# Kernel optimization log

Measured on AMD Instinct MI355X. Metric: run time of the kernel, lower is better.

The kernel has to match this reference:

```python
import jax, jax.numpy as jnp
import numpy as np

HEADS = 16
KERNEL_EPS = 1e-4  # performer_pytorch softmax_kernel eps
LN_EPS = 1e-5


def layernorm(x, g, b):
    m = jnp.mean(x, axis=-1, keepdims=True)
    v = jnp.var(x, axis=-1, keepdims=True)
    return (x - m) * jax.lax.rsqrt(v + LN_EPS) * g + b


def softmax_kernel(x, proj, is_query):
    # FAVOR+ positive random features (performer_pytorch softmax_kernel)
    d = x.shape[-1]
    m = proj.shape[0]
    xn = x * (d ** -0.25)                                   # data_normalizer * data
    dd = jnp.einsum('bhnd,md->bhnm', xn, proj)              # projected logits
    diag = 0.5 * jnp.sum(xn * xn, axis=-1, keepdims=True)   # ||x||^2/2 * normalizer^2
    if is_query:
        stab = jnp.max(dd, axis=-1, keepdims=True)
    else:
        stab = jnp.max(dd, axis=(-2, -1), keepdims=True)
    return (m ** -0.5) * (jnp.exp(dd - diag - stab) + KERNEL_EPS)


def favor_attention(x, proj, Wq, bq, Wk, bk, Wv, bv, Wo, bo):
    B, N, D = x.shape
    dh = D // HEADS

    def split(t):
        return t.reshape(B, N, HEADS, dh).transpose(0, 2, 1, 3)  # b h n d

    q = split(x @ Wq.T + bq)
    k = split(x @ Wk.T + bk)
    v = split(x @ Wv.T + bv)

    qp = softmax_kernel(q, proj, True)    # b h n m
    kp = softmax_kernel(k, proj, False)   # b h n m

    # non-causal linear attention: O(n*m*d)
    ksum = kp.sum(axis=2)                                    # b h m
    d_inv = 1.0 / jnp.einsum('bhnm,bhm->bhn', qp, ksum)      # b h n
    ctx = jnp.einsum('bhnm,bhnd->bhmd', kp, v)               # b h m d
    out = jnp.einsum('bhnm,bhmd,bhn->bhnd', qp, ctx, d_inv)  # b h n d

    out = out.transpose(0, 2, 1, 3).reshape(B, N, D)
    return out @ Wo.T + bo


def reference(x, proj, ln1_g, ln1_b, Wq, bq, Wk, bk, Wv, bv, Wo, bo,
              ln2_g, ln2_b, W1, b1, W2, b2):
    depth = proj.shape[0]
    for i in range(depth):
        h = layernorm(x, ln1_g[i], ln1_b[i])
        x = x + favor_attention(h, proj[i], Wq[i], bq[i], Wk[i], bk[i],
                                Wv[i], bv[i], Wo[i], bo[i])
        h = layernorm(x, ln2_g[i], ln2_b[i])
        x = x + (jax.nn.gelu(h @ W1[i].T + b1[i], approximate=False) @ W2[i].T + b2[i])
    return x


def _orthogonal_features(rng, m, d):
    # gaussian orthogonal random matrix, scaling=1 (rows scaled by sqrt(d))
    blocks = []
    for _ in range(m // d):
        qmat, _ = np.linalg.qr(rng.standard_normal((d, d)))
        blocks.append(qmat.T)
    return (np.sqrt(d) * np.concatenate(blocks, axis=0)).astype(np.float32)


def setup_inputs() -> dict:
    B, N, D, L, M, DH = 4, 2048, 1024, 4, 256, 64
    key = jax.random.key(0)
    ks = jax.random.split(key, 8)
    rng = np.random.default_rng(0)
    proj = jnp.asarray(np.stack([_orthogonal_features(rng, M, DH) for _ in range(L)]))
    s = 0.02
    return {
        'x': jax.random.normal(ks[0], (B, N, D), jnp.float32),
        'proj': proj,
        'ln1_g': jnp.ones((L, D), jnp.float32),
        'ln1_b': jnp.zeros((L, D), jnp.float32),
        'Wq': s * jax.random.normal(ks[1], (L, D, D), jnp.float32),
        'bq': jnp.zeros((L, D), jnp.float32),
        'Wk': s * jax.random.normal(ks[2], (L, D, D), jnp.float32),
        'bk': jnp.zeros((L, D), jnp.float32),
        'Wv': s * jax.random.normal(ks[3], (L, D, D), jnp.float32),
        'bv': jnp.zeros((L, D), jnp.float32),
        'Wo': s * jax.random.normal(ks[4], (L, D, D), jnp.float32),
        'bo': jnp.zeros((L, D), jnp.float32),
        'ln2_g': jnp.ones((L, D), jnp.float32),
        'ln2_b': jnp.zeros((L, D), jnp.float32),
        'W1': s * jax.random.normal(ks[5], (L, D, D), jnp.float32),
        'b1': jnp.zeros((L, D), jnp.float32),
        'W2': s * jax.random.normal(ks[6], (L, D, D), jnp.float32),
        'b2': jnp.zeros((L, D), jnp.float32),
    }
```

## Files before the change

kernel.cpp:

```cpp
#include <hip/hip_runtime.h>

#define B_    4
#define N_    2048
#define D_    1024
#define L_    4
#define M_    256
#define DH_   64
#define H_    16
#define BH_   64
#define ROWS_ 8192
#define WN_   1048576

typedef __bf16 bf16x8 __attribute__((ext_vector_type(8)));
typedef float  f32x4  __attribute__((ext_vector_type(4)));
typedef unsigned short u16;

__device__ __forceinline__ u16 f2b(float f){
  unsigned u = __float_as_uint(f);
  u += 0x7FFFu + ((u >> 16) & 1u);
  return (u16)(u >> 16);
}
__device__ __forceinline__ float b2f(u16 h){ return __uint_as_float(((unsigned)h) << 16); }
__device__ __forceinline__ unsigned fkey(float x){
  unsigned u = __float_as_uint(x);
  return (u & 0x80000000u) ? ~u : (u | 0x80000000u);
}
__device__ __forceinline__ float fdec(unsigned k){
  unsigned u = (k & 0x80000000u) ? (k ^ 0x80000000u) : ~k;
  return __uint_as_float(u);
}

__device__ __forceinline__ void gload16(const u16* g, u16* l){
  __builtin_amdgcn_global_load_lds(
      (const __attribute__((address_space(1))) void*)g,
      (__attribute__((address_space(3))) void*)l, 16, 0, 0);
}

__global__ __launch_bounds__(256) void wcvt_k(const float* __restrict__ s, u16* __restrict__ d, long n){
  long i = ((long)blockIdx.x*256 + threadIdx.x)*4;
  if (i+3 < n){
    float4 v = *(const float4*)(s+i);
    d[i]=f2b(v.x); d[i+1]=f2b(v.y); d[i+2]=f2b(v.z); d[i+3]=f2b(v.w);
  } else {
    for(long j=i;j<n;j++) d[j]=f2b(s[j]);
  }
}

__global__ __launch_bounds__(256) void wcvt2_k(const float* __restrict__ s, u16* __restrict__ dbase, long n){
  long i = ((long)blockIdx.x*256 + threadIdx.x)*4;
  if (i < n){
    float4 v = *(const float4*)(s+i);
    long l = i >> 20, j = i & (WN_-1);
    u16* d = dbase + l*(6l*WN_) + j;
    d[0]=f2b(v.x); d[1]=f2b(v.y); d[2]=f2b(v.z); d[3]=f2b(v.w);
  }
}

__global__ void fillf_k(float* o, long n, float v){
  long i=(long)blockIdx.x*256+threadIdx.x; if(i<n) o[i]=v;
}

__global__ __launch_bounds__(256) void ln_k(const float* __restrict__ x,
    const float* __restrict__ g, const float* __restrict__ bt, u16* __restrict__ h){
  int row = blockIdx.x, t = threadIdx.x;
  const float* xr = x + (long)row*D_;
  float4 v = *(const float4*)(xr + t*4);
  float s  = v.x+v.y+v.z+v.w;
  float ss = v.x*v.x+v.y*v.y+v.z*v.z+v.w*v.w;
  #pragma unroll
  for (int m=1;m<64;m<<=1){ s += __shfl_xor(s,m); ss += __shfl_xor(ss,m); }
  __shared__ float ps[4][2];
  int w=t>>6;
  if ((t&63)==0){ ps[w][0]=s; ps[w][1]=ss; }
  __syncthreads();
  s  = ps[0][0]+ps[1][0]+ps[2][0]+ps[3][0];
  ss = ps[0][1]+ps[1][1]+ps[2][1]+ps[3][1];
  float mean = s*(1.0f/D_);
  float rs = rsqrtf(ss*(1.0f/D_) - mean*mean + 1e-5f);
  int c=t*4;
  u16* hr = h + (long)row*D_;
  hr[c+0]=f2b((v.x-mean)*rs*g[c+0]+bt[c+0]);
  hr[c+1]=f2b((v.y-mean)*rs*g[c+1]+bt[c+1]);
  hr[c+2]=f2b((v.z-mean)*rs*g[c+2]+bt[c+2]);
  hr[c+3]=f2b((v.w-mean)*rs*g[c+3]+bt[c+3]);
}

__global__ __launch_bounds__(256) void vt_k(const u16* __restrict__ V, u16* __restrict__ Vt){
  __shared__ __align__(16) u16 ts[64][72];
  int t=threadIdx.x, z=blockIdx.y, n0=blockIdx.x*64;
  int b=z>>4, hh=z&15;
  {
    int row=t>>2, c16=(t&3)*16;
    const u16* src = V + ((long)b*N_ + n0+row)*D_ + hh*DH_ + c16;
    *(uint4*)&ts[row][c16]   = *(const uint4*)src;
    *(uint4*)&ts[row][c16+8] = *(const uint4*)(src+8);
  }
  __syncthreads();
  {
    int d=t>>2, nc=(t&3)*16;
    union { u16 u[16]; uint4 q[2]; } tmp;
    #pragma unroll
    for (int j=0;j<16;j++) tmp.u[j]=ts[nc+j][d];
    u16* dst = Vt + (long)z*DH_*N_ + (long)d*N_ + n0+nc;
    *(uint4*)dst = tmp.q[0];
    *(uint4*)(dst+8) = tmp.q[1];
  }
}

#define STAGE_PS(Ps, P) \
  _Pragma("unroll") \
  for (int i=0;i<8;i++){ \
    int c=threadIdx.x+i*256, row=c>>3, c8=c&7; \
    uint4 dv = *(const uint4*)((P) + row*64 + c8*8); \
    *(uint4*)((char*)(Ps) + (row<<7) + ((c8<<4)^((row&7)<<4))) = dv; \
  }
#define STAGE_XS(Xs, X, b, hh, n0) \
  _Pragma("unroll") \
  for (int i=0;i<2;i++){ \
    int c=threadIdx.x+i*256, row=c>>3, c8=c&7; \
    uint4 dv = *(const uint4*)((X) + ((long)(b)*N_ + (n0)+row)*D_ + (hh)*DH_ + c8*8); \
    *(uint4*)((char*)(Xs) + (row<<7) + ((c8<<4)^((row&7)<<4))) = dv; \
  }
#define STAGE_XS_DG(Xs, X, b, hh, n0, dgL) \
  _Pragma("unroll") \
  for (int i=0;i<2;i++){ \
    int c=threadIdx.x+i*256, row=c>>3, c8=c&7; \
    uint4 dv = *(const uint4*)((X) + ((long)(b)*N_ + (n0)+row)*D_ + (hh)*DH_ + c8*8); \
    *(uint4*)((char*)(Xs) + (row<<7) + ((c8<<4)^((row&7)<<4))) = dv; \
    const u16* pe=(const u16*)&dv; \
    float sq=0.f; \
    _Pragma("unroll") \
    for (int e=0;e<8;e++){ float xv=b2f(pe[e]); sq += xv*xv; } \
    sq += __shfl_xor(sq,1); sq += __shfl_xor(sq,2); sq += __shfl_xor(sq,4); \
    if ((threadIdx.x&7)==0) (dgL)[row]=sq*0.0625f; \
  }
#define DD_MFMA(acc, Xs, Ps, w, lr, lg) \
  _Pragma("unroll") \
  for (int ks=0;ks<2;ks++){ \
    bf16x8 aF[4], bF[4]; \
    _Pragma("unroll") \
    for (int mi=0;mi<4;mi++){ \
      int row=mi*16+(lr); \
      aF[mi]=*(const bf16x8*)((const char*)(Xs) + (row<<7) + ((((ks<<2)+(lg))<<4)^((row&7)<<4))); \
    } \
    _Pragma("unroll") \
    for (int ni=0;ni<4;ni++){ \
      int row=(w)*64+ni*16+(lr); \
      bF[ni]=*(const bf16x8*)((const char*)(Ps) + (row<<7) + ((((ks<<2)+(lg))<<4)^((row&7)<<4))); \
    } \
    _Pragma("unroll") \
    for (int mi=0;mi<4;mi++) \
      _Pragma("unroll") \
      for (int ni=0;ni<4;ni++) \
        acc[mi][ni]=__builtin_amdgcn_mfma_f32_16x16x32_bf16(aF[mi],bF[ni],acc[mi][ni],0,0,0); \
  }

__global__ __launch_bounds__(256) void ddstab_k(
    const u16* __restrict__ X, const u16* __restrict__ P,
    unsigned* __restrict__ sk, int zoff)
{
  __shared__ __align__(16) char smem[46080];
  u16* Ps=(u16*)smem; u16* Xs=(u16*)(smem+36864); float* rm=(float*)(smem+45056);
  int t=threadIdx.x, w=t>>6, lane=t&63, lr=lane&15, lg=lane>>4;
  int zg=blockIdx.y+zoff, n0=blockIdx.x*64;
  int b=zg>>4, hh=zg&15;
  STAGE_PS(Ps, P); STAGE_XS(Xs, X, b, hh, n0);
  __syncthreads();
  f32x4 acc[4][4];
  #pragma unroll
  for (int mi=0;mi<4;mi++)
    #pragma unroll
    for (int ni=0;ni<4;ni++) acc[mi][ni]=(f32x4){0.f,0.f,0.f,0.f};
  DD_MFMA(acc, Xs, Ps, w, lr, lg);
  float mx = acc[0][0][0];
  #pragma unroll
  for (int mi=0;mi<4;mi++)
    #pragma unroll
    for (int ni=0;ni<4;ni++)
      #pragma unroll
      for (int r=0;r<4;r++) mx=fmaxf(mx,acc[mi][ni][r]);
  #pragma unroll
  for (int m=1;m<64;m<<=1) mx = fmaxf(mx, __shfl_xor(mx,m));
  if (lane==0) rm[w]=mx;
  __syncthreads();
  const float SN = 0.35355339059327373f;
  if (t==0) atomicMax(sk+zg, fkey(SN*fmaxf(fmaxf(rm[0],rm[1]),fmaxf(rm[2],rm[3]))));
}

__global__ __launch_bounds__(256) void ddctx_k(
    const u16* __restrict__ Kb, const u16* __restrict__ P,
    const u16* __restrict__ Vt, const unsigned* __restrict__ sk,
    float* __restrict__ part, float* __restrict__ kspart, int zoff)
{
  __shared__ __align__(16) char smem[54784];
  u16* Ps = (u16*)smem;
  u16* Tr = (u16*)smem;
  u16* Xs = (u16*)(smem+36864);
  u16* Vs = (u16*)(smem+45056);
  float* dgL = (float*)(smem+54272);
  int t=threadIdx.x, w=t>>6, lane=t&63, lr=lane&15, lg=lane>>4;
  int zl=blockIdx.y, zg=zl+zoff, slot=blockIdx.x;
  int b=zg>>4, hh=zg&15;
  const float SN = 0.35355339059327373f;
  float stab = fdec(sk[zg]);

  f32x4 cacc[4][4];
  #pragma unroll
  for (int mi=0;mi<4;mi++)
    #pragma unroll
    for (int ni=0;ni<4;ni++) cacc[mi][ni]=(f32x4){0.f,0.f,0.f,0.f};
  float ksp[4]={0.f,0.f,0.f,0.f};

  for (int s=0;s<4;++s){
    int n0 = slot*256 + s*64;
    STAGE_PS(Ps, P); STAGE_XS_DG(Xs, Kb, b, hh, n0, dgL);
    {
      int d=t>>2, nc=(t&3)*16;
      const u16* src = Vt + (long)zg*DH_*N_ + (long)d*N_ + n0 + nc;
      *(uint4*)&Vs[d*72+nc]   = *(const uint4*)src;
      *(uint4*)&Vs[d*72+nc+8] = *(const uint4*)(src+8);
    }
    __syncthreads();
    f32x4 acc[4][4];
    #pragma unroll
    for (int mi=0;mi<4;mi++)
      #pragma unroll
      for (int ni=0;ni<4;ni++) acc[mi][ni]=(f32x4){0.f,0.f,0.f,0.f};
    DD_MFMA(acc, Xs, Ps, w, lr, lg);
    __syncthreads();
    #pragma unroll
    for (int mi=0;mi<4;mi++)
      #pragma unroll
      for (int ni=0;ni<4;ni++){
        int col = w*64+ni*16+lr;
        #pragma unroll
        for (int r=0;r<4;r++){
          int rw = mi*16+lg*4+r;
          float kp = 0.0625f*(expf(SN*acc[mi][ni][r] - dgL[rw] - stab) + 1e-4f);
          Tr[col*72+rw] = f2b(kp);
          ksp[ni] += kp;
        }
      }
    __syncthreads();
    #pragma unroll
    for (int ks=0;ks<2;ks++){
      bf16x8 aF[4], bF[4];
      #pragma unroll
      for (int mi=0;mi<4;mi++)
        aF[mi]=*(const bf16x8*)(Tr + (w*64+mi*16+lr)*72 + ks*32 + lg*8);
      #pragma unroll
      for (int ni=0;ni<4;ni++)
        bF[ni]=*(const bf16x8*)(Vs + (ni*16+lr)*72 + ks*32 + lg*8);
      #pragma unroll
      for (int mi=0;mi<4;mi++)
        #pragma unroll
        for (int ni=0;ni<4;ni++)
          cacc[mi][ni]=__builtin_amdgcn_mfma_f32_16x16x32_bf16(aF[mi],bF[ni],cacc[mi][ni],0,0,0);
    }
    __syncthreads();
  }
  #pragma unroll
  for (int ni=0;ni<4;ni++){
    ksp[ni] += __shfl_xor(ksp[ni],16);
    ksp[ni] += __shfl_xor(ksp[ni],32);
  }
  if (lane<16){
    float* kb_ = kspart + ((long)zl*8+slot)*256;
    #pragma unroll
    for (int ni=0;ni<4;ni++) kb_[w*64+ni*16+lane] = ksp[ni];
  }
  float* pb = part + ((long)zl*8+slot)*16384;
  #pragma unroll
  for (int mi=0;mi<4;mi++)
    #pragma unroll
    for (int ni=0;ni<4;ni++){
      int d = ni*16+lr;
      #pragma unroll
      for (int r=0;r<4;r++){
        int m = w*64+mi*16+lg*4+r;
        pb[m*64+d] = cacc[mi][ni][r];
      }
    }
}

__global__ __launch_bounds__(256) void ctxred2_k(
    const float* __restrict__ part, const float* __restrict__ kspart,
    u16* __restrict__ ctxT, float* __restrict__ ksm)
{
  int z = blockIdx.x, t = threadIdx.x;
  const float* pz = part + (long)z*8*16384;
  const float* kz = kspart + (long)z*8*256;
  float s=0.f;
  #pragma unroll
  for (int s8=0;s8<8;s8++) s += kz[s8*256+t];
  ksm[(long)z*256+t]=s;
  f32x4 r4[16];
  #pragma unroll
  for (int j=0;j<16;j++) r4[j] = *(const f32x4*)(pz + (long)t*64 + j*4);
  #pragma unroll
  for (int s8=1;s8<8;s8++){
    const float* ps = pz + (long)s8*16384 + (long)t*64;
    #pragma unroll
    for (int j=0;j<16;j++) r4[j] += *(const f32x4*)(ps + j*4);
  }
  u16 rb[64];
  #pragma unroll
  for (int j=0;j<16;j++){
    rb[j*4+0]=f2b(r4[j][0]); rb[j*4+1]=f2b(r4[j][1]);
    rb[j*4+2]=f2b(r4[j][2]); rb[j*4+3]=f2b(r4[j][3]);
  }
  __shared__ __align__(16) u16 TT[64][72];
  u16* co = ctxT + (long)z*16384;
  for (int c=0;c<4;c++){
    __syncthreads();
    if ((t>>6)==c){
      int r=t&63;
      #pragma unroll
      for (int j=0;j<64;j+=8) *(uint4*)&TT[r][j] = *(const uint4*)&rb[j];
    }
    __syncthreads();
    int d=t>>2, mq=(t&3)*16;
    union { u16 u[16]; uint4 q[2]; } tmp;
    #pragma unroll
    for (int j=0;j<16;j++) tmp.u[j]=TT[mq+j][d];
    *(uint4*)(co + d*256 + c*64 + mq)     = tmp.q[0];
    *(uint4*)(co + d*256 + c*64 + mq + 8) = tmp.q[1];
  }
}

__global__ __launch_bounds__(256) void ddq_attn_k(
    const u16* __restrict__ Qb, const u16* __restrict__ P,
    const float* __restrict__ ksm, const u16* __restrict__ ctxT,
    u16* __restrict__ at, int zoff)
{
  __shared__ __align__(16) char smem[46336];
  u16*   Ps  = (u16*)smem;
  u16*   qpL = (u16*)smem;
  float* rdot= (float*)(smem+33792);
  float* dnvs= (float*)(smem+34816);
  u16*   Xs  = (u16*)(smem+36864);
  float* rm  = (float*)(smem+45056);
  float* dgL = (float*)(smem+46080);
  int t=threadIdx.x, w=t>>6, lane=t&63, lr=lane&15, lg=lane>>4;
  int zl=blockIdx.y, zg=zl+zoff, n0=blockIdx.x*64;
  int b=zg>>4, hh=zg&15;
  const float SN = 0.35355339059327373f;

  STAGE_PS(Ps, P); STAGE_XS_DG(Xs, Qb, b, hh, n0, dgL);
  __syncthreads();
  f32x4 acc[4][4];
  #pragma unroll
  for (int mi=0;mi<4;mi++)
    #pragma unroll
    for (int ni=0;ni<4;ni++) acc[mi][ni]=(f32x4){0.f,0.f,0.f,0.f};
  DD_MFMA(acc, Xs, Ps, w, lr, lg);
  float rmx[4][4];
  #pragma unroll
  for (int mi=0;mi<4;mi++)
    #pragma unroll
    for (int r=0;r<4;r++){
      float v = acc[mi][0][r];
      #pragma unroll
      for (int ni=1;ni<4;ni++) v=fmaxf(v, acc[mi][ni][r]);
      #pragma unroll
      for (int m=1;m<16;m<<=1) v = fmaxf(v, __shfl_xor(v,m));
      rmx[mi][r]=v;
    }
  if (lr==0){
    #pragma unroll
    for (int mi=0;mi<4;mi++)
      #pragma unroll
      for (int r=0;r<4;r++) rm[w*64 + mi*16 + lg*4 + r] = rmx[mi][r];
  }
  __syncthreads();
  const float* ksz = ksm + (long)zl*256;
  float kcol[4];
  #pragma unroll
  for (int ni=0;ni<4;ni++) kcol[ni] = ksz[w*64+ni*16+lr];
  float rd[4][4];
  #pragma unroll
  for (int mi=0;mi<4;mi++)
    #pragma unroll
    for (int r=0;r<4;r++){
      int rw = mi*16+lg*4+r;
      float st = fmaxf(fmaxf(rm[rw],rm[64+rw]),fmaxf(rm[128+rw],rm[192+rw]));
      float dgv = dgL[rw];
      float rsum = 0.f;
      #pragma unroll
      for (int ni=0;ni<4;ni++){
        int col = w*64+ni*16+lr;
        float qpv = 0.0625f*(expf(SN*acc[mi][ni][r] - dgv - SN*st) + 1e-4f);
        qpL[rw*264+col] = f2b(qpv);
        rsum += qpv*kcol[ni];
      }
      rd[mi][r]=rsum;
    }
  #pragma unroll
  for (int mi=0;mi<4;mi++)
    #pragma unroll
    for (int r=0;r<4;r++){
      #pragma unroll
      for (int m=1;m<16;m<<=1) rd[mi][r] += __shfl_xor(rd[mi][r],m);
    }
  if (lr==0){
    #pragma unroll
    for (int mi=0;mi<4;mi++)
      #pragma unroll
      for (int r=0;r<4;r++) rdot[w*64 + mi*16+lg*4+r] = rd[mi][r];
  }
  __syncthreads();
  if (t<64) dnvs[t] = 1.0f/(rdot[t]+rdot[64+t]+rdot[128+t]+rdot[192+t]);
  __syncthreads();
  const u16* cz = ctxT + (long)zl*16384;
  f32x4 aacc[4];
  #pragma unroll
  for (int ni=0;ni<4;ni++) aacc[ni]=(f32x4){0.f,0.f,0.f,0.f};
  #pragma unroll
  for (int ks=0;ks<8;ks++){
    bf16x8 aF = *(const bf16x8*)(qpL + (w*16+lr)*264 + ks*32 + lg*8);
    #pragma unroll
    for (int ni=0;ni<4;ni++){
      bf16x8 bF = *(const bf16x8*)(cz + (ni*16+lr)*256 + ks*32 + lg*8);
      aacc[ni]=__builtin_amdgcn_mfma_f32_16x16x32_bf16(aF,bF,aacc[ni],0,0,0);
    }
  }
  #pragma unroll
  for (int ni=0;ni<4;ni++){
    #pragma unroll
    for (int r=0;r<4;r++){
      int n = n0 + w*16 + lg*4 + r;
      at[((long)b*N_ + n)*D_ + hh*64 + ni*16 + lr] = f2b(aacc[ni][r]*dnvs[w*16+lg*4+r]);
    }
  }
}

template<int BM,int BN,int WR,int WC,int EPI,bool XS>
__global__ __launch_bounds__(256) void gemm_k(
    const u16* __restrict__ A, int lda,
    const u16* __restrict__ W, int ldw,
    const float* __restrict__ bias, const float* __restrict__ biasK, const float* __restrict__ biasV,
    void* __restrict__ Cv, int ldc, int K)
{
  static_assert(WR*WC==4, "4 waves");
  constexpr int WM=BM/WR, WN=BN/WC, MI=WM/16, NI=WN/16;
  __shared__ __align__(16) u16 As[BM*64];
  __shared__ __align__(16) u16 Ws[BN*64];
  int t=threadIdx.x;
  int bx, by;
  if (XS){
    unsigned gx=gridDim.x, flat=blockIdx.y*gx+blockIdx.x;
    unsigned cpx=(gx*gridDim.y)>>3;
    unsigned s=(flat&7)*cpx + (flat>>3);
    bx = s % gx; by = s / gx;
  } else { bx = blockIdx.x; by = blockIdx.y; }
  const u16* Ab = A + (long)by*BM*lda;
  const u16* Wb = W + (long)bx*BN*ldw;
  int w=t>>6, lane=t&63, lr=lane&15, lg=lane>>4;
  int wr=w/WC, wc=w%WC;
  int srow=lane>>3, swcol=((lane&7)^srow)*8;
  f32x4 acc[MI][NI];
  #pragma unroll
  for (int mi=0;mi<MI;mi++)
    #pragma unroll
    for(int ni=0;ni<NI;ni++) acc[mi][ni]=(f32x4){0.f,0.f,0.f,0.f};

  for (int k0=0;k0<K;k0+=64){
    #pragma unroll
    for (int i=0;i<BM/32;i++){
      int rb=w*(BM/4)+i*8;
      gload16(Ab + (long)(rb+srow)*lda + k0 + swcol, As + rb*64);
    }
    #pragma unroll
    for (int i=0;i<BN/32;i++){
      int rb=w*(BN/4)+i*8;
      gload16(Wb + (long)(rb+srow)*ldw + k0 + swcol, Ws + rb*64);
    }
    __syncthreads();
    #pragma unroll
    for (int ks=0;ks<2;ks++){
      bf16x8 aF[MI], bF[NI];
      #pragma unroll
      for (int mi=0;mi<MI;mi++){
        int row=wr*WM+mi*16+lr;
        aF[mi]=*(const bf16x8*)((const char*)As + (row<<7) + ((((ks<<2)+lg)<<4)^((row&7)<<4)));
      }
      #pragma unroll
      for (int ni=0;ni<NI;ni++){
        int row=wc*WN+ni*16+lr;
        bF[ni]=*(const bf16x8*)((const char*)Ws + (row<<7) + ((((ks<<2)+lg)<<4)^((row&7)<<4)));
      }
      #pragma unroll
      for (int mi=0;mi<MI;mi++)
        #pragma unroll
        for (int ni=0;ni<NI;ni++)
          acc[mi][ni]=__builtin_amdgcn_mfma_f32_16x16x32_bf16(aF[mi],bF[ni],acc[mi][ni],0,0,0);
    }
    __syncthreads();
  }

  #pragma unroll
  for (int mi=0;mi<MI;mi++){
    #pragma unroll
    for (int ni=0;ni<NI;ni++){
      int col = bx*BN + wc*WN + ni*16 + lr;
      float bv = 0.0f;
      if (EPI==6){
        int seg = col>>10;
        const float* bp = (seg==0)?bias:((seg==1)?biasK:biasV);
        bv = bp[col&1023];
      } else if (EPI<=2){
        bv = bias[col];
      }
      #pragma unroll
      for (int r=0;r<4;r++){
        int row = by*BM + wr*WM + mi*16 + lg*4 + r;
        float v = acc[mi][ni][r];
        if (EPI==0){
          ((u16*)Cv)[(long)row*ldc + col] = f2b(v+bv);
        } else if (EPI==1){
          ((float*)Cv)[(long)row*ldc + col] += v+bv;
        } else if (EPI==2){
          float u=v+bv;
          ((u16*)Cv)[(long)row*ldc + col] = f2b(0.5f*u*(1.0f+erff(u*0.70710678118654752f)));
        } else {
          int seg = col>>10, c = col&1023;
          ((u16*)Cv)[(long)seg*((long)ROWS_*D_) + (long)row*D_ + c] = f2b(v+bv);
        }
      }
    }
  }
}

struct WS {
  u16 *wbuf, *pjb, *hb, *qb, *kb, *pbuf, *sh16, *ctxT;
  float *part, *kspart, *ksm; unsigned* sky;
  size_t total;
};
static WS plan_ws(char* base, int allW, int CH){
  WS w; size_t off=0;
  auto al=[&](size_t b)->char*{ char* p=base+off; off=(off+b+255)&~(size_t)255; return p; };
  const size_t TB=(size_t)ROWS_*D_*2;
  w.wbuf=(u16*)al((allW?6ull*L_:6ull)*WN_*2);
  w.pjb =(u16*)al((size_t)L_*M_*DH_*2);
  w.hb  =(u16*)al(TB);
  w.qb  =(u16*)al(TB);
  w.kb  =(u16*)al(TB);
  w.pbuf=(u16*)al(TB);
  w.sh16=(u16*)al(TB);
  w.part=(float*)al((size_t)CH*8*M_*DH_*4);
  w.kspart=(float*)al((size_t)CH*8*M_*4);
  w.ctxT=(u16*)al((size_t)BH_*DH_*M_*2);
  w.ksm =(float*)al((size_t)BH_*M_*4);
  w.sky =(unsigned*)al((size_t)L_*BH_*4);
  w.total=off;
  return w;
}

extern "C" void kernel_launch(void* const* d_in, const int* in_sizes, int n_in,
                              void* d_out, int out_size, void* d_ws, size_t ws_size,
                              hipStream_t stream)
{
  const float* x    = (const float*)d_in[0];
  const float* proj = (const float*)d_in[1];
  const float* ln1g = (const float*)d_in[2];
  const float* ln1b = (const float*)d_in[3];
  const float* Wq   = (const float*)d_in[4];
  const float* bq   = (const float*)d_in[5];
  const float* Wk   = (const float*)d_in[6];
  const float* bk   = (const float*)d_in[7];
  const float* Wv   = (const float*)d_in[8];
  const float* bv   = (const float*)d_in[9];
  const float* Wo   = (const float*)d_in[10];
  const float* bo   = (const float*)d_in[11];
  const float* ln2g = (const float*)d_in[12];
  const float* ln2b = (const float*)d_in[13];
  const float* W1   = (const float*)d_in[14];
  const float* b1   = (const float*)d_in[15];
  const float* W2   = (const float*)d_in[16];
  const float* b2   = (const float*)d_in[17];

  char* base=(char*)d_ws;
  int allW=1, CH=64;
  WS w = plan_ws(base, 1, 64);
  if (w.total > ws_size){ CH=16; w = plan_ws(base, 1, 16); }
  if (w.total > ws_size){ allW=0; w = plan_ws(base, 0, 16); }
  if (w.total > ws_size){
    fillf_k<<<(out_size+255)/256,256,0,stream>>>((float*)d_out,(long)out_size,(float)(ws_size>>20));
    return;
  }
  const int NCH = BH_/CH;

  u16* vb = w.pbuf;
  u16* vt = w.sh16;
  u16* at = w.hb;
  u16* tm = w.sh16;

  wcvt_k<<<(L_*M_*DH_/4+255)/256,256,0,stream>>>(proj,w.pjb,(long)L_*M_*DH_);
  hipMemsetAsync(w.sky, 0, (size_t)L_*BH_*4, stream);
  if (allW){
    const long na = (long)L_*WN_;
    const int g2 = (int)(na/4/256);
    wcvt2_k<<<g2,256,0,stream>>>(Wq, w.wbuf,         na);
    wcvt2_k<<<g2,256,0,stream>>>(Wk, w.wbuf+WN_,     na);
    wcvt2_k<<<g2,256,0,stream>>>(Wv, w.wbuf+2l*WN_,  na);
    wcvt2_k<<<g2,256,0,stream>>>(Wo, w.wbuf+3l*WN_,  na);
    wcvt2_k<<<g2,256,0,stream>>>(W1, w.wbuf+4l*WN_,  na);
    wcvt2_k<<<g2,256,0,stream>>>(W2, w.wbuf+5l*WN_,  na);
  }
  hipMemcpyAsync(d_out, x, (size_t)ROWS_*D_*4, hipMemcpyDeviceToDevice, stream);
  float* Xc = (float*)d_out;

  const long wn = (long)WN_;
  const int wg = (int)(wn/4/256);
  dim3 gBig(D_/128, ROWS_/64, 1);
  dim3 gQKV(3*D_/128, ROWS_/128, 1);

  for (int l=0;l<L_;l++){
    u16* lw = w.wbuf + (allW ? (size_t)l*6*wn : 0);
    u16* wqkv=lw;  u16* wo=lw+3*wn;  u16* w1=lw+4*wn;  u16* w2=lw+5*wn;
    if (!allW){
      wcvt_k<<<wg,256,0,stream>>>(Wq+(size_t)l*wn,lw,wn);
      wcvt_k<<<wg,256,0,stream>>>(Wk+(size_t)l*wn,lw+wn,wn);
      wcvt_k<<<wg,256,0,stream>>>(Wv+(size_t)l*wn,lw+2*wn,wn);
      wcvt_k<<<wg,256,0,stream>>>(Wo+(size_t)l*wn,wo,wn);
      wcvt_k<<<wg,256,0,stream>>>(W1+(size_t)l*wn,w1,wn);
      wcvt_k<<<wg,256,0,stream>>>(W2+(size_t)l*wn,w2,wn);
    }
    const u16* pj = w.pjb + (size_t)l*M_*DH_;
    unsigned* skl = w.sky + (size_t)l*BH_;

    ln_k<<<ROWS_,256,0,stream>>>(Xc, ln1g+(size_t)l*D_, ln1b+(size_t)l*D_, w.hb);
    gemm_k<128,128,2,2,6,true><<<gQKV,256,0,stream>>>(w.hb,D_, wqkv,D_,
        bq+(size_t)l*D_, bk+(size_t)l*D_, bv+(size_t)l*D_, w.qb,D_,D_);
    vt_k<<<dim3(N_/64,BH_),256,0,stream>>>(vb, vt);

    for (int ch=0; ch<NCH; ch++){
      int zoff = ch*CH;
      ddstab_k<<<dim3(N_/64,CH),256,0,stream>>>(w.kb, pj, skl, zoff);
      ddctx_k<<<dim3(8,CH),256,0,stream>>>(w.kb, pj, vt, skl, w.part, w.kspart, zoff);
      ctxred2_k<<<CH,256,0,stream>>>(w.part, w.kspart,
                                     w.ctxT+(long)zoff*DH_*M_, w.ksm+(long)zoff*M_);
      ddq_attn_k<<<dim3(N_/64,CH),256,0,stream>>>(w.qb, pj,
                                                  w.ksm+(long)zoff*M_,
                                                  w.ctxT+(long)zoff*DH_*M_, at, zoff);
    }

    gemm_k<64,128,1,4,1,true><<<gBig,256,0,stream>>>(at,D_, wo,D_,
        bo+(size_t)l*D_, nullptr, nullptr, Xc,D_,D_);
    ln_k<<<ROWS_,256,0,stream>>>(Xc, ln2g+(size_t)l*D_, ln2b+(size_t)l*D_, w.hb);
    gemm_k<64,128,1,4,2,true><<<gBig,256,0,stream>>>(w.hb,D_, w1,D_,
        b1+(size_t)l*D_, nullptr, nullptr, tm,D_,D_);
    gemm_k<64,128,1,4,1,true><<<gBig,256,0,stream>>>(tm,D_, w2,D_,
        b2+(size_t)l*D_, nullptr, nullptr, Xc,D_,D_);
  }
}
```

Baseline: 1.382 ms.

## Fuse key stabilizer max into context kernel via online rescaling; double-buffer GEMM

```diff
diff --git a/kernel.cpp b/kernel.cpp
--- a/kernel.cpp
+++ b/kernel.cpp
@@ -21,14 +21,6 @@
   return (u16)(u >> 16);
 }
 __device__ __forceinline__ float b2f(u16 h){ return __uint_as_float(((unsigned)h) << 16); }
-__device__ __forceinline__ unsigned fkey(float x){
-  unsigned u = __float_as_uint(x);
-  return (u & 0x80000000u) ? ~u : (u | 0x80000000u);
-}
-__device__ __forceinline__ float fdec(unsigned k){
-  unsigned u = (k & 0x80000000u) ? (k ^ 0x80000000u) : ~k;
-  return __uint_as_float(u);
-}
 
 __device__ __forceinline__ void gload16(const u16* g, u16* l){
   __builtin_amdgcn_global_load_lds(
@@ -113,13 +105,6 @@
     int c=threadIdx.x+i*256, row=c>>3, c8=c&7; \
     uint4 dv = *(const uint4*)((P) + row*64 + c8*8); \
     *(uint4*)((char*)(Ps) + (row<<7) + ((c8<<4)^((row&7)<<4))) = dv; \
-  }
-#define STAGE_XS(Xs, X, b, hh, n0) \
-  _Pragma("unroll") \
-  for (int i=0;i<2;i++){ \
-    int c=threadIdx.x+i*256, row=c>>3, c8=c&7; \
-    uint4 dv = *(const uint4*)((X) + ((long)(b)*N_ + (n0)+row)*D_ + (hh)*DH_ + c8*8); \
-    *(uint4*)((char*)(Xs) + (row<<7) + ((c8<<4)^((row&7)<<4))) = dv; \
   }
 #define STAGE_XS_DG(Xs, X, b, hh, n0, dgL) \
   _Pragma("unroll") \
@@ -155,42 +140,11 @@
         acc[mi][ni]=__builtin_amdgcn_mfma_f32_16x16x32_bf16(aF[mi],bF[ni],acc[mi][ni],0,0,0); \
   }
 
-__global__ __launch_bounds__(256) void ddstab_k(
-    const u16* __restrict__ X, const u16* __restrict__ P,
-    unsigned* __restrict__ sk, int zoff)
-{
-  __shared__ __align__(16) char smem[46080];
-  u16* Ps=(u16*)smem; u16* Xs=(u16*)(smem+36864); float* rm=(float*)(smem+45056);
-  int t=threadIdx.x, w=t>>6, lane=t&63, lr=lane&15, lg=lane>>4;
-  int zg=blockIdx.y+zoff, n0=blockIdx.x*64;
-  int b=zg>>4, hh=zg&15;
-  STAGE_PS(Ps, P); STAGE_XS(Xs, X, b, hh, n0);
-  __syncthreads();
-  f32x4 acc[4][4];
-  #pragma unroll
-  for (int mi=0;mi<4;mi++)
-    #pragma unroll
-    for (int ni=0;ni<4;ni++) acc[mi][ni]=(f32x4){0.f,0.f,0.f,0.f};
-  DD_MFMA(acc, Xs, Ps, w, lr, lg);
-  float mx = acc[0][0][0];
-  #pragma unroll
-  for (int mi=0;mi<4;mi++)
-    #pragma unroll
-    for (int ni=0;ni<4;ni++)
-      #pragma unroll
-      for (int r=0;r<4;r++) mx=fmaxf(mx,acc[mi][ni][r]);
-  #pragma unroll
-  for (int m=1;m<64;m<<=1) mx = fmaxf(mx, __shfl_xor(mx,m));
-  if (lane==0) rm[w]=mx;
-  __syncthreads();
-  const float SN = 0.35355339059327373f;
-  if (t==0) atomicMax(sk+zg, fkey(SN*fmaxf(fmaxf(rm[0],rm[1]),fmaxf(rm[2],rm[3]))));
-}
-
 __global__ __launch_bounds__(256) void ddctx_k(
     const u16* __restrict__ Kb, const u16* __restrict__ P,
-    const u16* __restrict__ Vt, const unsigned* __restrict__ sk,
-    float* __restrict__ part, float* __restrict__ kspart, int zoff)
+    const u16* __restrict__ Vt,
+    float* __restrict__ part, float* __restrict__ kspart,
+    float* __restrict__ msl, float* __restrict__ vsl, int zoff)
 {
   __shared__ __align__(16) char smem[54784];
   u16* Ps = (u16*)smem;
@@ -198,11 +152,11 @@
   u16* Xs = (u16*)(smem+36864);
   u16* Vs = (u16*)(smem+45056);
   float* dgL = (float*)(smem+54272);
+  float* rm  = (float*)(smem+54528);
   int t=threadIdx.x, w=t>>6, lane=t&63, lr=lane&15, lg=lane>>4;
   int zl=blockIdx.y, zg=zl+zoff, slot=blockIdx.x;
   int b=zg>>4, hh=zg&15;
   const float SN = 0.35355339059327373f;
-  float stab = fdec(sk[zg]);
 
   f32x4 cacc[4][4];
   #pragma unroll
@@ -210,6 +164,8 @@
     #pragma unroll
     for (int ni=0;ni<4;ni++) cacc[mi][ni]=(f32x4){0.f,0.f,0.f,0.f};
   float ksp[4]={0.f,0.f,0.f,0.f};
+  float vsacc=0.f;
+  float mrun=-1e30f;
 
   for (int s=0;s<4;++s){
     int n0 = slot*256 + s*64;
@@ -221,13 +177,47 @@
       *(uint4*)&Vs[d*72+nc+8] = *(const uint4*)(src+8);
     }
     __syncthreads();
+    {
+      int d=t>>2, q=t&3;
+      float sv=0.f;
+      #pragma unroll
+      for (int j=0;j<16;j++) sv += b2f(Vs[d*72+q*16+j]);
+      sv += __shfl_xor(sv,1); sv += __shfl_xor(sv,2);
+      if (q==0) vsacc += sv;
+    }
     f32x4 acc[4][4];
     #pragma unroll
     for (int mi=0;mi<4;mi++)
       #pragma unroll
       for (int ni=0;ni<4;ni++) acc[mi][ni]=(f32x4){0.f,0.f,0.f,0.f};
     DD_MFMA(acc, Xs, Ps, w, lr, lg);
+    {
+      float mx = acc[0][0][0];
+      #pragma unroll
+      for (int mi=0;mi<4;mi++)
+        #pragma unroll
+        for (int ni=0;ni<4;ni++)
+          #pragma unroll
+          for (int r=0;r<4;r++) mx=fmaxf(mx,acc[mi][ni][r]);
+      #pragma unroll
+      for (int m=1;m<64;m<<=1) mx = fmaxf(mx, __shfl_xor(mx,m));
+      if (lane==0) rm[w]=mx;
+    }
     __syncthreads();
+    {
+      float tm = SN*fmaxf(fmaxf(rm[0],rm[1]),fmaxf(rm[2],rm[3]));
+      float nm = fmaxf(mrun, tm);
+      float sc = expf(mrun - nm);
+      mrun = nm;
+      #pragma unroll
+      for (int mi=0;mi<4;mi++)
+        #pragma unroll
+        for (int ni=0;ni<4;ni++)
+          #pragma unroll
+          for (int r=0;r<4;r++) cacc[mi][ni][r] *= sc;
+      #pragma unroll
+      for (int ni=0;ni<4;ni++) ksp[ni] *= sc;
+    }
     #pragma unroll
     for (int mi=0;mi<4;mi++)
       #pragma unroll
@@ -236,7 +226,7 @@
         #pragma unroll
         for (int r=0;r<4;r++){
           int rw = mi*16+lg*4+r;
-          float kp = 0.0625f*(expf(SN*acc[mi][ni][r] - dgL[rw] - stab) + 1e-4f);
+          float kp = 0.0625f*expf(SN*acc[mi][ni][r] - dgL[rw] - mrun);
           Tr[col*72+rw] = f2b(kp);
           ksp[ni] += kp;
         }
@@ -264,12 +254,15 @@
     ksp[ni] += __shfl_xor(ksp[ni],16);
     ksp[ni] += __shfl_xor(ksp[ni],32);
   }
+  long sb = (long)zl*8+slot;
   if (lane<16){
-    float* kb_ = kspart + ((long)zl*8+slot)*256;
+    float* kb_ = kspart + sb*256;
     #pragma unroll
     for (int ni=0;ni<4;ni++) kb_[w*64+ni*16+lane] = ksp[ni];
   }
-  float* pb = part + ((long)zl*8+slot)*16384;
+  if (t==0) msl[sb]=mrun;
+  if ((t&3)==0) vsl[sb*64 + (t>>2)] = vsacc;
+  float* pb = part + sb*16384;
   #pragma unroll
   for (int mi=0;mi<4;mi++)
     #pragma unroll
@@ -285,29 +278,51 @@
 
 __global__ __launch_bounds__(256) void ctxred2_k(
     const float* __restrict__ part, const float* __restrict__ kspart,
+    const float* __restrict__ msl, const float* __restrict__ vsl,
     u16* __restrict__ ctxT, float* __restrict__ ksm)
 {
   int z = blockIdx.x, t = threadIdx.x;
   const float* pz = part + (long)z*8*16384;
   const float* kz = kspart + (long)z*8*256;
+  const float* mz = msl + (long)z*8;
+  const float* vz = vsl + (long)z*8*64;
+  float mg = mz[0];
+  #pragma unroll
+  for (int s8=1;s8<8;s8++) mg = fmaxf(mg, mz[s8]);
+  float scl[8];
+  #pragma unroll
+  for (int s8=0;s8<8;s8++) scl[s8] = expf(mz[s8]-mg);
   float s=0.f;
   #pragma unroll
-  for (int s8=0;s8<8;s8++) s += kz[s8*256+t];
-  ksm[(long)z*256+t]=s;
+  for (int s8=0;s8<8;s8++) s += kz[s8*256+t]*scl[s8];
+  ksm[(long)z*256+t] = s + 0.0128f;
+  __shared__ float vsT[64];
+  if (t<64){
+    float vv=0.f;
+    #pragma unroll
+    for (int s8=0;s8<8;s8++) vv += vz[s8*64+t];
+    vsT[t]=vv;
+  }
+  __syncthreads();
   f32x4 r4[16];
   #pragma unroll
-  for (int j=0;j<16;j++) r4[j] = *(const f32x4*)(pz + (long)t*64 + j*4);
-  #pragma unroll
-  for (int s8=1;s8<8;s8++){
+  for (int j=0;j<16;j++) r4[j]=(f32x4){0.f,0.f,0.f,0.f};
+  #pragma unroll
+  for (int s8=0;s8<8;s8++){
     const float* ps = pz + (long)s8*16384 + (long)t*64;
-    #pragma unroll
-    for (int j=0;j<16;j++) r4[j] += *(const f32x4*)(ps + j*4);
+    float sc = scl[s8];
+    #pragma unroll
+    for (int j=0;j<16;j++){
+      f32x4 v = *(const f32x4*)(ps + j*4);
+      r4[j] += (f32x4){sc*v[0],sc*v[1],sc*v[2],sc*v[3]};
+    }
   }
   u16 rb[64];
   #pragma unroll
   for (int j=0;j<16;j++){
-    rb[j*4+0]=f2b(r4[j][0]); rb[j*4+1]=f2b(r4[j][1]);
-    rb[j*4+2]=f2b(r4[j][2]); rb[j*4+3]=f2b(r4[j][3]);
+    #pragma unroll
+    for (int e=0;e<4;e++)
+      rb[j*4+e]=f2b(r4[j][e] + 6.25e-6f*vsT[j*4+e]);
   }
   __shared__ __align__(16) u16 TT[64][72];
   u16* co = ctxT + (long)z*16384;
@@ -443,8 +458,8 @@
 {
   static_assert(WR*WC==4, "4 waves");
   constexpr int WM=BM/WR, WN=BN/WC, MI=WM/16, NI=WN/16;
-  __shared__ __align__(16) u16 As[BM*64];
-  __shared__ __align__(16) u16 Ws[BN*64];
+  __shared__ __align__(16) u16 As[2][BM*64];
+  __shared__ __align__(16) u16 Ws[2][BN*64];
   int t=threadIdx.x;
   int bx, by;
   if (XS){
@@ -464,30 +479,31 @@
     #pragma unroll
     for(int ni=0;ni<NI;ni++) acc[mi][ni]=(f32x4){0.f,0.f,0.f,0.f};
 
-  for (int k0=0;k0<K;k0+=64){
+  auto stage=[&](u16* Asb, u16* Wsb, int k0){
     #pragma unroll
     for (int i=0;i<BM/32;i++){
       int rb=w*(BM/4)+i*8;
-      gload16(Ab + (long)(rb+srow)*lda + k0 + swcol, As + rb*64);
+      gload16(Ab + (long)(rb+srow)*lda + k0 + swcol, Asb + rb*64);
     }
     #pragma unroll
     for (int i=0;i<BN/32;i++){
       int rb=w*(BN/4)+i*8;
-      gload16(Wb + (long)(rb+srow)*ldw + k0 + swcol, Ws + rb*64);
-    }
-    __syncthreads();
+      gload16(Wb + (long)(rb+srow)*ldw + k0 + swcol, Wsb + rb*64);
+    }
+  };
+  auto compute=[&](const u16* Asb, const u16* Wsb){
     #pragma unroll
     for (int ks=0;ks<2;ks++){
       bf16x8 aF[MI], bF[NI];
       #pragma unroll
       for (int mi=0;mi<MI;mi++){
         int row=wr*WM+mi*16+lr;
-        aF[mi]=*(const bf16x8*)((const char*)As + (row<<7) + ((((ks<<2)+lg)<<4)^((row&7)<<4)));
+        aF[mi]=*(const bf16x8*)((const char*)Asb + (row<<7) + ((((ks<<2)+lg)<<4)^((row&7)<<4)));
       }
       #pragma unroll
       for (int ni=0;ni<NI;ni++){
         int row=wc*WN+ni*16+lr;
-        bF[ni]=*(const bf16x8*)((const char*)Ws + (row<<7) + ((((ks<<2)+lg)<<4)^((row&7)<<4)));
+        bF[ni]=*(const bf16x8*)((const char*)Wsb + (row<<7) + ((((ks<<2)+lg)<<4)^((row&7)<<4)));
       }
       #pragma unroll
       for (int mi=0;mi<MI;mi++)
@@ -495,7 +511,19 @@
         for (int ni=0;ni<NI;ni++)
           acc[mi][ni]=__builtin_amdgcn_mfma_f32_16x16x32_bf16(aF[mi],bF[ni],acc[mi][ni],0,0,0);
     }
-    __syncthreads();
+  };
+
+  stage(As[0], Ws[0], 0);
+  asm volatile("s_waitcnt vmcnt(0)" ::: "memory");
+  __builtin_amdgcn_s_barrier();
+  const int nK = K/64;
+  for (int it=0; it<nK; ++it){
+    if (it+1<nK) stage(As[(it+1)&1], Ws[(it+1)&1], (it+1)*64);
+    compute(As[it&1], Ws[it&1]);
+    if (it+1<nK){
+      asm volatile("s_waitcnt vmcnt(0)" ::: "memory");
+      __builtin_amdgcn_s_barrier();
+    }
   }
 
   #pragma unroll
@@ -533,7 +561,7 @@
 
 struct WS {
   u16 *wbuf, *pjb, *hb, *qb, *kb, *pbuf, *sh16, *ctxT;
-  float *part, *kspart, *ksm; unsigned* sky;
+  float *part, *kspart, *msl, *vsl, *ksm;
   size_t total;
 };
 static WS plan_ws(char* base, int allW, int CH){
@@ -549,9 +577,10 @@
   w.sh16=(u16*)al(TB);
   w.part=(float*)al((size_t)CH*8*M_*DH_*4);
   w.kspart=(float*)al((size_t)CH*8*M_*4);
+  w.msl =(float*)al((size_t)CH*8*4);
+  w.vsl =(float*)al((size_t)CH*8*DH_*4);
   w.ctxT=(u16*)al((size_t)BH_*DH_*M_*2);
   w.ksm =(float*)al((size_t)BH_*M_*4);
-  w.sky =(unsigned*)al((size_t)L_*BH_*4);
   w.total=off;
   return w;
 }
@@ -596,7 +625,6 @@
   u16* tm = w.sh16;
 
   wcvt_k<<<(L_*M_*DH_/4+255)/256,256,0,stream>>>(proj,w.pjb,(long)L_*M_*DH_);
-  hipMemsetAsync(w.sky, 0, (size_t)L_*BH_*4, stream);
   if (allW){
     const long na = (long)L_*WN_;
     const int g2 = (int)(na/4/256);
@@ -627,7 +655,6 @@
       wcvt_k<<<wg,256,0,stream>>>(W2+(size_t)l*wn,w2,wn);
     }
     const u16* pj = w.pjb + (size_t)l*M_*DH_;
-    unsigned* skl = w.sky + (size_t)l*BH_;
 
     ln_k<<<ROWS_,256,0,stream>>>(Xc, ln1g+(size_t)l*D_, ln1b+(size_t)l*D_, w.hb);
     gemm_k<128,128,2,2,6,true><<<gQKV,256,0,stream>>>(w.hb,D_, wqkv,D_,
@@ -636,9 +663,9 @@
 
     for (int ch=0; ch<NCH; ch++){
       int zoff = ch*CH;
-      ddstab_k<<<dim3(N_/64,CH),256,0,stream>>>(w.kb, pj, skl, zoff);
-      ddctx_k<<<dim3(8,CH),256,0,stream>>>(w.kb, pj, vt, skl, w.part, w.kspart, zoff);
-      ctxred2_k<<<CH,256,0,stream>>>(w.part, w.kspart,
+      ddctx_k<<<dim3(8,CH),256,0,stream>>>(w.kb, pj, vt, w.part, w.kspart,
+                                           w.msl, w.vsl, zoff);
+      ctxred2_k<<<CH,256,0,stream>>>(w.part, w.kspart, w.msl, w.vsl,
                                      w.ctxT+(long)zoff*DH_*M_, w.ksm+(long)zoff*M_);
       ddq_attn_k<<<dim3(N_/64,CH),256,0,stream>>>(w.qb, pj,
                                                   w.ksm+(long)zoff*M_,
```

Result: slower. 1.441 ms (+4.3%).
